# Kernel optimization log

Measured on AMD Instinct MI355X. Metric: run time of the kernel, lower is better.

Reference implementation:

```python
import jax, jax.numpy as jnp
import numpy as np


def setup_inputs() -> dict:
    key = jax.random.key(0)
    k1, k2, k3, k4 = jax.random.split(key, 4)
    B, R, S = 4, 8192, 32
    INPUT_DIM, SLOT_DIM, ATT_DIM = 180, 1536, 1536
    x = jax.random.normal(k1, (B, R, INPUT_DIM), dtype=jnp.float32)
    slot_latents = jax.random.normal(k2, (B, S, SLOT_DIM), dtype=jnp.float32)
    # Linear weights (no bias), stored as [in, out]
    Wq = jax.random.normal(k3, (INPUT_DIM, ATT_DIM), dtype=jnp.float32) * (INPUT_DIM ** -0.5)
    Wk = jax.random.normal(k4, (SLOT_DIM, ATT_DIM), dtype=jnp.float32) * (SLOT_DIM ** -0.5)
    return {"x": x, "slot_latents": slot_latents, "Wq": Wq, "Wk": Wk}


def reference(x, slot_latents, Wq, Wk):
    # q: [B, R, A], k: [B, S, A]
    q = jnp.einsum('bri,ia->bra', x, Wq)
    k = jnp.einsum('bsi,ia->bsa', slot_latents, Wk)
    scale = Wq.shape[1] ** -0.5  # att_dim^{-1/2}
    dots = jnp.einsum('bra,bsa->brs', q, k) * scale
    w = jax.nn.softmax(dots, axis=2)  # softmax over slots
    # Weighted sum of raw slot_latents (V = slot_latents), fused as a matmul
    # instead of materializing the [B, R, S, slot_dim] broadcast intermediate.
    s = jnp.einsum('brs,bsd->brd', w, slot_latents)
    return (s, w)
```

## Files before the change

### kernel.cpp

```cpp
#include <hip/hip_runtime.h>
#include <math.h>

#define BB 4
#define RR 8192
#define SS 32
#define IN_DIM 180
#define SLOT_DIM 1536
#define ATT 1536

__global__ __launch_bounds__(256) void k_proj_kernel(const float* __restrict__ slot,
                                                     const float* __restrict__ Wk,
                                                     float* __restrict__ k_ws) {
    const int ICH = 384;
    __shared__ __align__(16) float sl[BB * ICH];
    const int s  = blockIdx.x;
    const int a0 = blockIdx.y * 256;
    const int i0 = blockIdx.z * ICH;
    const int t  = threadIdx.x;

    for (int idx = t; idx < BB * ICH; idx += 256) {
        int b = idx / ICH, ii = idx - b * ICH;
        sl[idx] = slot[((size_t)(b * SS + s)) * SLOT_DIM + i0 + ii];
    }
    __syncthreads();

    float acc0 = 0.f, acc1 = 0.f, acc2 = 0.f, acc3 = 0.f;
    const int a = a0 + t;
    const float* wkp = Wk + (size_t)i0 * ATT + a;
#pragma unroll 8
    for (int ii = 0; ii < ICH; ++ii) {
        float wk = wkp[(size_t)ii * ATT];
        acc0 += sl[0 * ICH + ii] * wk;
        acc1 += sl[1 * ICH + ii] * wk;
        acc2 += sl[2 * ICH + ii] * wk;
        acc3 += sl[3 * ICH + ii] * wk;
    }
    atomicAdd(&k_ws[((size_t)(0 * SS + s)) * ATT + a], acc0);
    atomicAdd(&k_ws[((size_t)(1 * SS + s)) * ATT + a], acc1);
    atomicAdd(&k_ws[((size_t)(2 * SS + s)) * ATT + a], acc2);
    atomicAdd(&k_ws[((size_t)(3 * SS + s)) * ATT + a], acc3);
}

__global__ __launch_bounds__(256) void m_kernel(const float* __restrict__ Wq,
                                                const float* __restrict__ k_ws,
                                                float* __restrict__ M_ws) {
    __shared__ __align__(16) float kr[ATT];
    const int bs = blockIdx.x;
    const int b = bs / SS, s = bs - b * SS;
    const int t = threadIdx.x;

    for (int idx = t; idx < ATT; idx += 256) kr[idx] = k_ws[(size_t)bs * ATT + idx];
    __syncthreads();

    const int wave = t >> 6, lane = t & 63;
    const int i = blockIdx.y * 4 + wave;
    const float scale = 0.0255155181f;

    const float* wq = Wq + (size_t)i * ATT;
    float p = 0.f;
#pragma unroll
    for (int j = 0; j < ATT / 64; ++j) {
        int a = lane + j * 64;
        p += wq[a] * kr[a];
    }
    for (int m = 32; m >= 1; m >>= 1) p += __shfl_xor(p, m, 64);
    if (lane == 0) M_ws[((size_t)b * IN_DIM + i) * SS + s] = p * scale;
}

__global__ __launch_bounds__(256) void attn_w_kernel(const float* __restrict__ x,
                                                     const float* __restrict__ M_ws,
                                                     float* __restrict__ w_out) {
    const int TR = 32;
    __shared__ __align__(16) float xs[TR * IN_DIM];
    __shared__ __align__(16) float Ms[IN_DIM * SS];
    __shared__ __align__(16) float wt[TR * 33];
    const int b  = blockIdx.y;
    const int r0 = blockIdx.x * TR;
    const int t  = threadIdx.x;

    {
        const float4* src = (const float4*)(x + ((size_t)b * RR + r0) * IN_DIM);
        float4* dst = (float4*)xs;
        for (int idx = t; idx < TR * IN_DIM / 4; idx += 256) dst[idx] = src[idx];
    }
    {
        const float4* src = (const float4*)(M_ws + (size_t)b * IN_DIM * SS);
        float4* dst = (float4*)Ms;
        for (int idx = t; idx < IN_DIM * SS / 4; idx += 256) dst[idx] = src[idx];
    }
    __syncthreads();

    const int r = t >> 3, sq = (t & 7) * 4;
    float a0 = 0.f, a1 = 0.f, a2 = 0.f, a3 = 0.f;
#pragma unroll 4
    for (int i = 0; i < IN_DIM; ++i) {
        float xv = xs[r * IN_DIM + i];
        const float4 m4 = *(const float4*)(Ms + i * SS + sq);
        a0 += xv * m4.x; a1 += xv * m4.y; a2 += xv * m4.z; a3 += xv * m4.w;
    }
    wt[r * 33 + sq + 0] = a0;
    wt[r * 33 + sq + 1] = a1;
    wt[r * 33 + sq + 2] = a2;
    wt[r * 33 + sq + 3] = a3;
    __syncthreads();

    if (t < TR) {
        float mx = -1e30f;
#pragma unroll
        for (int j = 0; j < SS; ++j) mx = fmaxf(mx, wt[t * 33 + j]);
        float sum = 0.f;
#pragma unroll
        for (int j = 0; j < SS; ++j) {
            float e = __expf(wt[t * 33 + j] - mx);
            wt[t * 33 + j] = e;
            sum += e;
        }
        float inv = 1.0f / sum;
#pragma unroll
        for (int j = 0; j < SS; ++j) wt[t * 33 + j] *= inv;
    }
    __syncthreads();

    float* wg = w_out + ((size_t)b * RR + r0) * SS;
    for (int idx = t; idx < TR * SS; idx += 256) {
        int rr = idx >> 5, ss = idx & 31;
        wg[idx] = wt[rr * 33 + ss];
    }
}

__global__ __launch_bounds__(256) void out_kernel(const float* __restrict__ slot,
                                                  const float* __restrict__ w_g,
                                                  float* __restrict__ out) {
    const int TRO = 64, TD = 256;
    __shared__ __align__(16) float wt[TRO * SS];
    __shared__ __align__(16) float st[SS * TD];
    const int b  = blockIdx.z;
    const int r0 = blockIdx.x * TRO;
    const int d0 = blockIdx.y * TD;
    const int t  = threadIdx.x;

    {
        const float4* src = (const float4*)(w_g + ((size_t)b * RR + r0) * SS);
        float4* dst = (float4*)wt;
        for (int idx = t; idx < TRO * SS / 4; idx += 256) dst[idx] = src[idx];
    }
#pragma unroll 4
    for (int ss = 0; ss < SS; ++ss) {
        st[ss * TD + t] = slot[((size_t)b * SS + ss) * SLOT_DIM + d0 + t];
    }
    __syncthreads();

    const int dq = (t & 63) * 4, rg = (t >> 6) * 16;
    float4 acc[16];
#pragma unroll
    for (int r = 0; r < 16; ++r) acc[r] = make_float4(0.f, 0.f, 0.f, 0.f);

    for (int ss = 0; ss < SS; ++ss) {
        const float4 v = *(const float4*)(st + ss * TD + dq);
#pragma unroll
        for (int r = 0; r < 16; ++r) {
            float wv = wt[(rg + r) * SS + ss];
            acc[r].x += wv * v.x;
            acc[r].y += wv * v.y;
            acc[r].z += wv * v.z;
            acc[r].w += wv * v.w;
        }
    }

#pragma unroll
    for (int r = 0; r < 16; ++r) {
        *(float4*)(out + ((size_t)b * RR + r0 + rg + r) * SLOT_DIM + d0 + dq) = acc[r];
    }
}

extern "C" void kernel_launch(void* const* d_in, const int* in_sizes, int n_in,
                              void* d_out, int out_size, void* d_ws, size_t ws_size,
                              hipStream_t stream) {
    const float* x    = (const float*)d_in[0];
    const float* slot = (const float*)d_in[1];
    const float* Wq   = (const float*)d_in[2];
    const float* Wk   = (const float*)d_in[3];

    float* out   = (float*)d_out;
    float* w_out = out + (size_t)BB * RR * SLOT_DIM;

    float* k_ws = (float*)d_ws;
    float* M_ws = k_ws + (size_t)BB * SS * ATT;

    hipMemsetAsync(k_ws, 0, (size_t)BB * SS * ATT * sizeof(float), stream);

    k_proj_kernel<<<dim3(SS, ATT / 256, SLOT_DIM / 384), 256, 0, stream>>>(slot, Wk, k_ws);
    m_kernel<<<dim3(BB * SS, IN_DIM / 4), 256, 0, stream>>>(Wq, k_ws, M_ws);
    attn_w_kernel<<<dim3(RR / 32, BB), 256, 0, stream>>>(x, M_ws, w_out);
    out_kernel<<<dim3(RR / 64, SLOT_DIM / 256, BB), 256, 0, stream>>>(slot, w_out, out);
}
```

Measured before the change: 304.3 us.

## Retile output GEMM with transposed weights and register blocking; rework projection kernels

out_kernel now stores the softmax weights transposed with padding and loads them as float4. Each thread computes an 8x8 register tile instead of 16 rows by 4 columns, and slot rows are staged with float4 loads. This is meant to raise arithmetic intensity and cut LDS traffic in the dominant output GEMM. attn_w_kernel handles 64 rows per block with two rows per thread and reads M directly from global memory instead of staging it in LDS. k_proj_kernel halves its input chunk and interleaves batches so one float4 LDS read serves all four batches, at the cost of twice as many atomics.

```diff
diff --git a/kernel.cpp b/kernel.cpp
--- a/kernel.cpp
+++ b/kernel.cpp
@@ -11,8 +11,8 @@
 __global__ __launch_bounds__(256) void k_proj_kernel(const float* __restrict__ slot,
                                                      const float* __restrict__ Wk,
                                                      float* __restrict__ k_ws) {
-    const int ICH = 384;
-    __shared__ __align__(16) float sl[BB * ICH];
+    const int ICH = 192;
+    __shared__ __align__(16) float sl[ICH * BB];
     const int s  = blockIdx.x;
     const int a0 = blockIdx.y * 256;
     const int i0 = blockIdx.z * ICH;
@@ -20,7 +20,7 @@
 
     for (int idx = t; idx < BB * ICH; idx += 256) {
         int b = idx / ICH, ii = idx - b * ICH;
-        sl[idx] = slot[((size_t)(b * SS + s)) * SLOT_DIM + i0 + ii];
+        sl[ii * BB + b] = slot[((size_t)(b * SS + s)) * SLOT_DIM + i0 + ii];
     }
     __syncthreads();
 
@@ -30,10 +30,11 @@
 #pragma unroll 8
     for (int ii = 0; ii < ICH; ++ii) {
         float wk = wkp[(size_t)ii * ATT];
-        acc0 += sl[0 * ICH + ii] * wk;
-        acc1 += sl[1 * ICH + ii] * wk;
-        acc2 += sl[2 * ICH + ii] * wk;
-        acc3 += sl[3 * ICH + ii] * wk;
+        const float4 s4 = *(const float4*)(sl + ii * BB);
+        acc0 += s4.x * wk;
+        acc1 += s4.y * wk;
+        acc2 += s4.z * wk;
+        acc3 += s4.w * wk;
     }
     atomicAdd(&k_ws[((size_t)(0 * SS + s)) * ATT + a], acc0);
     atomicAdd(&k_ws[((size_t)(1 * SS + s)) * ATT + a], acc1);
@@ -70,9 +71,8 @@
 __global__ __launch_bounds__(256) void attn_w_kernel(const float* __restrict__ x,
                                                      const float* __restrict__ M_ws,
                                                      float* __restrict__ w_out) {
-    const int TR = 32;
+    const int TR = 64;
     __shared__ __align__(16) float xs[TR * IN_DIM];
-    __shared__ __align__(16) float Ms[IN_DIM * SS];
     __shared__ __align__(16) float wt[TR * 33];
     const int b  = blockIdx.y;
     const int r0 = blockIdx.x * TR;
@@ -83,25 +83,26 @@
         float4* dst = (float4*)xs;
         for (int idx = t; idx < TR * IN_DIM / 4; idx += 256) dst[idx] = src[idx];
     }
-    {
-        const float4* src = (const float4*)(M_ws + (size_t)b * IN_DIM * SS);
-        float4* dst = (float4*)Ms;
-        for (int idx = t; idx < IN_DIM * SS / 4; idx += 256) dst[idx] = src[idx];
-    }
-    __syncthreads();
-
-    const int r = t >> 3, sq = (t & 7) * 4;
-    float a0 = 0.f, a1 = 0.f, a2 = 0.f, a3 = 0.f;
+    __syncthreads();
+
+    const float* Mg = M_ws + (size_t)b * IN_DIM * SS;
+    const int rp = t >> 3;
+    const int sq = (t & 7) * 4;
+    const int ra = rp * 2, rb = ra + 1;
+    float4 A = make_float4(0.f, 0.f, 0.f, 0.f);
+    float4 Bv = make_float4(0.f, 0.f, 0.f, 0.f);
 #pragma unroll 4
     for (int i = 0; i < IN_DIM; ++i) {
-        float xv = xs[r * IN_DIM + i];
-        const float4 m4 = *(const float4*)(Ms + i * SS + sq);
-        a0 += xv * m4.x; a1 += xv * m4.y; a2 += xv * m4.z; a3 += xv * m4.w;
-    }
-    wt[r * 33 + sq + 0] = a0;
-    wt[r * 33 + sq + 1] = a1;
-    wt[r * 33 + sq + 2] = a2;
-    wt[r * 33 + sq + 3] = a3;
+        float x0 = xs[ra * IN_DIM + i];
+        float x1 = xs[rb * IN_DIM + i];
+        const float4 m4 = *(const float4*)(Mg + i * SS + sq);
+        A.x += x0 * m4.x; A.y += x0 * m4.y; A.z += x0 * m4.z; A.w += x0 * m4.w;
+        Bv.x += x1 * m4.x; Bv.y += x1 * m4.y; Bv.z += x1 * m4.z; Bv.w += x1 * m4.w;
+    }
+    wt[ra * 33 + sq + 0] = A.x;  wt[ra * 33 + sq + 1] = A.y;
+    wt[ra * 33 + sq + 2] = A.z;  wt[ra * 33 + sq + 3] = A.w;
+    wt[rb * 33 + sq + 0] = Bv.x; wt[rb * 33 + sq + 1] = Bv.y;
+    wt[rb * 33 + sq + 2] = Bv.z; wt[rb * 33 + sq + 3] = Bv.w;
     __syncthreads();
 
     if (t < TR) {
@@ -131,8 +132,8 @@
 __global__ __launch_bounds__(256) void out_kernel(const float* __restrict__ slot,
                                                   const float* __restrict__ w_g,
                                                   float* __restrict__ out) {
-    const int TRO = 64, TD = 256;
-    __shared__ __align__(16) float wt[TRO * SS];
+    const int TRO = 64, TD = 256, WP = 68;
+    __shared__ __align__(16) float wtT[SS * WP];
     __shared__ __align__(16) float st[SS * TD];
     const int b  = blockIdx.z;
     const int r0 = blockIdx.x * TRO;
@@ -141,35 +142,55 @@
 
     {
         const float4* src = (const float4*)(w_g + ((size_t)b * RR + r0) * SS);
-        float4* dst = (float4*)wt;
-        for (int idx = t; idx < TRO * SS / 4; idx += 256) dst[idx] = src[idx];
-    }
-#pragma unroll 4
+#pragma unroll
+        for (int k = 0; k < 2; ++k) {
+            int idx = t + k * 256;
+            int rr = idx >> 3, ssq = (idx & 7) * 4;
+            float4 f = src[idx];
+            wtT[(ssq + 0) * WP + rr] = f.x;
+            wtT[(ssq + 1) * WP + rr] = f.y;
+            wtT[(ssq + 2) * WP + rr] = f.z;
+            wtT[(ssq + 3) * WP + rr] = f.w;
+        }
+    }
+#pragma unroll
+    for (int k = 0; k < 8; ++k) {
+        int idx = t + k * 256;
+        int row = idx >> 6, c4 = (idx & 63) * 4;
+        *(float4*)(st + row * TD + c4) =
+            *(const float4*)(slot + ((size_t)(b * SS + row)) * SLOT_DIM + d0 + c4);
+    }
+    __syncthreads();
+
+    const int d  = (t & 31) * 8;
+    const int rg = (t >> 5) * 8;
+    float4 acc[8][2];
+#pragma unroll
+    for (int r = 0; r < 8; ++r) {
+        acc[r][0] = make_float4(0.f, 0.f, 0.f, 0.f);
+        acc[r][1] = make_float4(0.f, 0.f, 0.f, 0.f);
+    }
+
     for (int ss = 0; ss < SS; ++ss) {
-        st[ss * TD + t] = slot[((size_t)b * SS + ss) * SLOT_DIM + d0 + t];
-    }
-    __syncthreads();
-
-    const int dq = (t & 63) * 4, rg = (t >> 6) * 16;
-    float4 acc[16];
-#pragma unroll
-    for (int r = 0; r < 16; ++r) acc[r] = make_float4(0.f, 0.f, 0.f, 0.f);
-
-    for (int ss = 0; ss < SS; ++ss) {
-        const float4 v = *(const float4*)(st + ss * TD + dq);
-#pragma unroll
-        for (int r = 0; r < 16; ++r) {
-            float wv = wt[(rg + r) * SS + ss];
-            acc[r].x += wv * v.x;
-            acc[r].y += wv * v.y;
-            acc[r].z += wv * v.z;
-            acc[r].w += wv * v.w;
+        const float4 v0 = *(const float4*)(st + ss * TD + d);
+        const float4 v1 = *(const float4*)(st + ss * TD + d + 4);
+        const float4 w0 = *(const float4*)(wtT + ss * WP + rg);
+        const float4 w1 = *(const float4*)(wtT + ss * WP + rg + 4);
+        const float wr[8] = {w0.x, w0.y, w0.z, w0.w, w1.x, w1.y, w1.z, w1.w};
+#pragma unroll
+        for (int r = 0; r < 8; ++r) {
+            acc[r][0].x += wr[r] * v0.x; acc[r][0].y += wr[r] * v0.y;
+            acc[r][0].z += wr[r] * v0.z; acc[r][0].w += wr[r] * v0.w;
+            acc[r][1].x += wr[r] * v1.x; acc[r][1].y += wr[r] * v1.y;
+            acc[r][1].z += wr[r] * v1.z; acc[r][1].w += wr[r] * v1.w;
         }
     }
 
 #pragma unroll
-    for (int r = 0; r < 16; ++r) {
-        *(float4*)(out + ((size_t)b * RR + r0 + rg + r) * SLOT_DIM + d0 + dq) = acc[r];
+    for (int r = 0; r < 8; ++r) {
+        float* base = out + ((size_t)b * RR + r0 + rg + r) * SLOT_DIM + d0 + d;
+        *(float4*)(base + 0) = acc[r][0];
+        *(float4*)(base + 4) = acc[r][1];
     }
 }
 
@@ -189,8 +210,8 @@
 
     hipMemsetAsync(k_ws, 0, (size_t)BB * SS * ATT * sizeof(float), stream);
 
-    k_proj_kernel<<<dim3(SS, ATT / 256, SLOT_DIM / 384), 256, 0, stream>>>(slot, Wk, k_ws);
+    k_proj_kernel<<<dim3(SS, ATT / 256, SLOT_DIM / 192), 256, 0, stream>>>(slot, Wk, k_ws);
     m_kernel<<<dim3(BB * SS, IN_DIM / 4), 256, 0, stream>>>(Wq, k_ws, M_ws);
-    attn_w_kernel<<<dim3(RR / 32, BB), 256, 0, stream>>>(x, M_ws, w_out);
+    attn_w_kernel<<<dim3(RR / 64, BB), 256, 0, stream>>>(x, M_ws, w_out);
     out_kernel<<<dim3(RR / 64, SLOT_DIM / 256, BB), 256, 0, stream>>>(slot, w_out, out);
 }
```

Result: no change. 300.8 us (-1.1%).
